# Kernel tuning notes

Measured on AMD Instinct MI355X. Metric: run time of the kernel, lower is better.

Reference implementation:

```python
import jax, jax.numpy as jnp
import numpy as np

# Static multi-scale feature pyramid shapes (value_shapes arg of MSDeformAttn.forward)
VALUE_SHAPES = ((80, 80), (40, 40), (20, 20), (10, 10))
N_HEADS, N_LEVELS, N_POINTS, D_MODEL = 8, 4, 4, 256


def setup_inputs() -> dict:
    key = jax.random.key(0)
    ks = jax.random.split(key, 11)
    bs, lq, d = 16, 1000, D_MODEL
    lv = sum(h * w for h, w in VALUE_SHAPES)  # 8500
    s = 0.02  # weight scale
    f32 = jnp.float32
    return {
        "query": jax.random.normal(ks[0], (bs, lq, d), f32),
        "refer_bbox": jax.random.uniform(ks[1], (bs, lq, 1, 4), f32),  # cxcywh in [0,1]
        "value": jax.random.normal(ks[2], (bs, lv, d), f32),
        "W_off": jax.random.normal(ks[3], (d, N_HEADS * N_LEVELS * N_POINTS * 2), f32) * s,
        "b_off": jax.random.normal(ks[4], (N_HEADS * N_LEVELS * N_POINTS * 2,), f32) * s,
        "W_attn": jax.random.normal(ks[5], (d, N_HEADS * N_LEVELS * N_POINTS), f32) * s,
        "b_attn": jax.random.normal(ks[6], (N_HEADS * N_LEVELS * N_POINTS,), f32) * s,
        "W_val": jax.random.normal(ks[7], (d, d), f32) * s,
        "b_val": jax.random.normal(ks[8], (d,), f32) * s,
        "W_out": jax.random.normal(ks[9], (d, d), f32) * s,
        "b_out": jax.random.normal(ks[10], (d,), f32) * s,
    }


def _bilinear_sample(v, x, y):
    """grid_sample(mode=bilinear, padding=zeros, align_corners=False) equivalent.
    v: [bs, H, W, nh, dh]; x, y: pixel-space coords [bs, lq, nh, P].
    Returns [bs, lq, nh, P, dh]."""
    bs, H, W, nh, dh = v.shape
    x0f = jnp.floor(x)
    y0f = jnp.floor(y)
    wx = x - x0f  # fractional weights
    wy = y - y0f
    x0 = x0f.astype(jnp.int32)
    y0 = y0f.astype(jnp.int32)
    x1, y1 = x0 + 1, y0 + 1
    b_idx = jnp.arange(bs)[:, None, None, None]
    h_idx = jnp.arange(nh)[None, None, :, None]

    def gather(yi, xi):
        valid = (xi >= 0) & (xi < W) & (yi >= 0) & (yi < H)
        xc = jnp.clip(xi, 0, W - 1)
        yc = jnp.clip(yi, 0, H - 1)
        val = v[b_idx, yc, xc, h_idx]  # [bs, lq, nh, P, dh]
        return val * valid[..., None].astype(v.dtype)

    return (gather(y0, x0) * ((1 - wx) * (1 - wy))[..., None]
            + gather(y0, x1) * (wx * (1 - wy))[..., None]
            + gather(y1, x0) * ((1 - wx) * wy)[..., None]
            + gather(y1, x1) * (wx * wy)[..., None])


def reference(query, refer_bbox, value, W_off, b_off, W_attn, b_attn, W_val, b_val, W_out, b_out):
    bs, lq, d = query.shape
    nh, L, P = N_HEADS, N_LEVELS, N_POINTS
    dh = d // nh

    # value projection
    v = value @ W_val + b_val  # [bs, lv, d]
    v = v.reshape(bs, -1, nh, dh)

    # sampling offsets and attention weights from query
    offsets = (query @ W_off + b_off).reshape(bs, lq, nh, L, P, 2)
    attn = (query @ W_attn + b_attn).reshape(bs, lq, nh, L * P)
    attn = jax.nn.softmax(attn, axis=-1).reshape(bs, lq, nh, L, P)

    # refer_bbox: [bs, lq, 1, 4] cxcywh; num_points == 4 branch
    add = offsets / P * refer_bbox[:, :, None, :, None, 2:] * 0.5
    loc = refer_bbox[:, :, None, :, None, :2] + add  # [bs, lq, nh, L, P, 2] in [0,1]

    out = jnp.zeros((bs, lq, nh, dh), query.dtype)
    start = 0
    for l, (H, W) in enumerate(VALUE_SHAPES):
        vl = v[:, start:start + H * W].reshape(bs, H, W, nh, dh)
        start += H * W
        ll = loc[:, :, :, l]  # [bs, lq, nh, P, 2]
        # normalized [0,1] -> pixel coords (align_corners=False): p = loc*size - 0.5
        x = ll[..., 0] * W - 0.5
        y = ll[..., 1] * H - 0.5
        sampled = _bilinear_sample(vl, x, y)  # [bs, lq, nh, P, dh]
        out = out + jnp.einsum('bqhpd,bqhp->bqhd', sampled, attn[:, :, :, l])

    out = out.reshape(bs, lq, d)
    return out @ W_out + b_out
```

## Files before the change

kernel.cpp:

```cpp
#include <hip/hip_runtime.h>
#include <cstdint>
#include <cstddef>


typedef unsigned short u16;
typedef u16 u16x8 __attribute__((ext_vector_type(8)));
typedef __bf16 bf16x8 __attribute__((ext_vector_type(8)));
typedef float f32x4 __attribute__((ext_vector_type(4)));

__device__ inline u16 f2bf(float f) {
  return __builtin_bit_cast(u16, (__bf16)f);
}

__device__ __forceinline__ void glds16(const void* g, void* l) {
  __builtin_amdgcn_global_load_lds(
      (const __attribute__((address_space(1))) void*)g,
      (__attribute__((address_space(3))) void*)l, 16, 0, 0);
}

__global__ __launch_bounds__(256) void wconv(
    const float* __restrict__ W0, const float* __restrict__ W1,
    const float* __restrict__ W2, const float* __restrict__ W3,
    u16* __restrict__ T0, u16* __restrict__ T1, u16* __restrict__ T2,
    u16* __restrict__ T3) {
  __shared__ u16 tile[64][65];
  const float* Ws[4] = {W0, W1, W2, W3};
  u16* Ts[4] = {T0, T1, T2, T3};
  const int Ns[4] = {256, 256, 128, 256};
  const int z = blockIdx.z;
  const int N = Ns[z];
  const int n0 = blockIdx.x * 64;
  if (n0 >= N) return;
  const int k0 = blockIdx.y * 64;
  const float* W = Ws[z];
  u16* Wt = Ts[z];
  const int tr = threadIdx.x >> 6;
  const int tc = threadIdx.x & 63;
#pragma unroll
  for (int r = 0; r < 64; r += 4)
    tile[r + tr][tc] = f2bf(W[(size_t)(k0 + r + tr) * N + n0 + tc]);
  __syncthreads();
#pragma unroll
  for (int r = 0; r < 64; r += 4)
    Wt[(size_t)(n0 + r + tr) * 256 + k0 + tc] = tile[tc][r + tr];
}

template <int WAVES, int NF, bool OUT_BF16>
__global__ __launch_bounds__(WAVES * 64, 1) void gemm_p2(
    const float* __restrict__ A, const u16* __restrict__ Wt,
    const float* __restrict__ bias, void* __restrict__ Cv,
    int M, int NT, int G) {
  constexpr int N = NF * 16;
  constexpr int TR = WAVES * 16;
  constexpr int STN = OUT_BF16 ? (NF / 2) : NF;
  __shared__ __align__(16) u16 Bls[N * 256];
  __shared__ __align__(16) float Asub[WAVES * 1024];
  const int wave = threadIdx.x >> 6;
  const int lane = threadIdx.x & 63;
  const int lr = lane & 15;
  const int lj = lane >> 4;

  constexpr int NI = NF * 8 / WAVES;
#pragma unroll
  for (int g = 0; g < NI; ++g) {
    int inst = wave * NI + g;
    int s2 = inst * 2 + (lane >> 5);
    int pc = lane & 31;
    int jc = pc ^ (s2 & 7);
    int c = (s2 & 15) * NF + (s2 >> 4);
    glds16((const char*)Wt + (size_t)c * 512 + (size_t)jc * 16,
           (char*)Bls + inst * 1024);
  }

  float bv[NF];
#pragma unroll
  for (int ni = 0; ni < NF; ++ni) bv[ni] = bias[lr * NF + ni];

  char* aw = (char*)Asub + wave * 4096;

  auto stageA = [&](int t, int s, int buf) {
#pragma unroll
    for (int i = 0; i < 2; ++i) {
      long row = (long)t * TR + wave * 16 + i * 8 + (lane >> 3);
      if (row > (long)M - 1) row = M - 1;
      int jc = (lane & 7) ^ (lane >> 3);
      glds16((const char*)A + row * 1024 + (size_t)s * 128 + (size_t)jc * 16,
             aw + buf * 2048 + i * 1024);
    }
  };

  stageA(blockIdx.x, 0, 0);
  stageA(blockIdx.x, 1, 1);
  __syncthreads();

  for (int t = blockIdx.x; t < NT; t += G) {
    f32x4 acc[NF] = {};
#pragma unroll
    for (int s = 0; s < 8; ++s) {
      if (s < 2) {
        if constexpr (STN == 8)
          asm volatile("s_waitcnt vmcnt(10)" ::: "memory");
        else
          asm volatile("s_waitcnt vmcnt(18)" ::: "memory");
      } else {
        asm volatile("s_waitcnt vmcnt(2)" ::: "memory");
      }
      const char* ab = aw + (s & 1) * 2048;
      const int sw = lr & 7;
      const int j0 = lj * 2;
      f32x4 a0 = *(const f32x4*)(ab + lr * 128 + ((j0 ^ sw) * 16));
      f32x4 a1 = *(const f32x4*)(ab + lr * 128 + (((j0 + 1) ^ sw) * 16));
      bf16x8 af;
      af[0] = (__bf16)a0[0]; af[1] = (__bf16)a0[1];
      af[2] = (__bf16)a0[2]; af[3] = (__bf16)a0[3];
      af[4] = (__bf16)a1[0]; af[5] = (__bf16)a1[1];
      af[6] = (__bf16)a1[2]; af[7] = (__bf16)a1[3];
#pragma unroll
      for (int ni = 0; ni < NF; ++ni) {
        int sl = ni * 16 + lr;
        int pc = (s * 4 + lj) ^ (sl & 7);
        bf16x8 b = __builtin_bit_cast(
            bf16x8, *(const u16x8*)((const char*)Bls + sl * 512 + pc * 16));
        acc[ni] = __builtin_amdgcn_mfma_f32_16x16x32_bf16(af, b, acc[ni],
                                                          0, 0, 0);
      }
      if (s < 6)
        stageA(t, s + 2, s & 1);
      else if (s == 6)
        stageA(t + G, 0, 0);
      else
        stageA(t + G, 1, 1);
    }
#pragma unroll
    for (int r = 0; r < 4; ++r) {
      long grow = (long)t * TR + wave * 16 + lj * 4 + r;
      if (grow >= M) continue;
      if (OUT_BF16) {
        bf16x8 lo, hi;
#pragma unroll
        for (int j = 0; j < 8; ++j) {
          lo[j] = (__bf16)(acc[j][r] + bv[j]);
          hi[j] = (__bf16)(acc[8 + j][r] + bv[8 + j]);
        }
        u16* pC = (u16*)Cv + grow * N + lr * NF;
        *(u16x8*)pC = __builtin_bit_cast(u16x8, lo);
        *(u16x8*)(pC + 8) = __builtin_bit_cast(u16x8, hi);
      } else {
#pragma unroll
        for (int q = 0; q < NF / 4; ++q) {
          f32x4 v;
#pragma unroll
          for (int j = 0; j < 4; ++j) v[j] = acc[q * 4 + j][r] + bv[q * 4 + j];
          *(f32x4*)((float*)Cv + grow * N + lr * NF + q * 4) = v;
        }
      }
    }
  }
}

__global__ __launch_bounds__(256, 4) void sample_fused(
    const float* __restrict__ Lgo, const float* __restrict__ Lga,
    const float* __restrict__ bbox, const u16* __restrict__ vbf,
    float* __restrict__ outs) {
  const int t = threadIdx.x;
  const int bi = blockIdx.x;
  const int xcd = bi & 7;
  const int j = bi >> 3;
  const int half = (j >= 125) ? 1 : 0;
  const int batch = xcd + 8 * half;
  const int qb = j - 125 * half;
  const int i0 = (batch * 125 + qb) * 8;

  __shared__ __align__(16) float sa[8 * 128];
  __shared__ __align__(16) int4 soff[1024];
  __shared__ __align__(16) float4 sw4[1024];
  __shared__ float sb[32];
  if (t < 32) sb[t] = bbox[(size_t)i0 * 4 + t];
  ((float4*)sa)[t] = ((const float4*)(Lga + (size_t)i0 * 128))[t];
  __syncthreads();
  if (t < 64) {
    int base = (t >> 3) * 128 + (t & 7) * 16;
    float mx = -3.0e38f;
#pragma unroll
    for (int k = 0; k < 16; ++k) mx = fmaxf(mx, sa[base + k]);
    float e[16];
    float s = 0.f;
#pragma unroll
    for (int k = 0; k < 16; ++k) {
      e[k] = __expf(sa[base + k] - mx);
      s += e[k];
    }
    float inv = 1.f / s;
#pragma unroll
    for (int k = 0; k < 16; ++k) sa[base + k] = e[k] * inv;
  }
  __syncthreads();
#pragma unroll
  for (int it = 0; it < 4; ++it) {
    int idx = it * 256 + t;
    int ql = idx >> 7;
    int rest = idx & 127;
    int h = rest >> 4;
    int pt = rest & 15;
    int l = pt >> 2;
    int W = 80 >> l;
    float offx = Lgo[(size_t)(i0 + ql) * 256 + h * 32 + pt * 2];
    float offy = Lgo[(size_t)(i0 + ql) * 256 + h * 32 + pt * 2 + 1];
    float xf = (sb[ql * 4 + 0] + offx * 0.125f * sb[ql * 4 + 2]) * (float)W - 0.5f;
    float yf = (sb[ql * 4 + 1] + offy * 0.125f * sb[ql * 4 + 3]) * (float)W - 0.5f;
    float aw = sa[ql * 128 + h * 16 + pt];
    float x0f = floorf(xf), y0f = floorf(yf);
    float wx = xf - x0f, wy = yf - y0f;
    int x0 = (int)x0f, y0 = (int)y0f;
    int x1 = x0 + 1, y1 = y0 + 1;
    float fx0 = (x0 >= 0 && x0 < W) ? 1.f : 0.f;
    float fx1 = (x1 >= 0 && x1 < W) ? 1.f : 0.f;
    float fy0 = (y0 >= 0 && y0 < W) ? 1.f : 0.f;
    float fy1 = (y1 >= 0 && y1 < W) ? 1.f : 0.f;
    int xc0 = min(max(x0, 0), W - 1), xc1 = min(max(x1, 0), W - 1);
    int yc0 = min(max(y0, 0), W - 1), yc1 = min(max(y1, 0), W - 1);
    int baseb = ((25600 - (25600 >> (2 * l))) / 3) * 512;
    int4 o;
    o.x = baseb + (yc0 * W + xc0) * 512;
    o.y = baseb + (yc0 * W + xc1) * 512;
    o.z = baseb + (yc1 * W + xc0) * 512;
    o.w = baseb + (yc1 * W + xc1) * 512;
    float aw0 = aw * (1.f - wy), aw1 = aw * wy;
    float4 wv;
    wv.x = aw0 * (1.f - wx) * fx0 * fy0;
    wv.y = aw0 * wx * fx1 * fy0;
    wv.z = aw1 * (1.f - wx) * fx0 * fy1;
    wv.w = aw1 * wx * fx1 * fy1;
    int phys = ql * 128 + h * 16 + (pt ^ h);
    soff[phys] = o;
    sw4[phys] = wv;
  }
  __syncthreads();
  const int ql = t >> 5;
  const int r = t & 31;
  const int h = r >> 2;
  const int cg = r & 3;
  const int chb = (h * 32 + cg * 8) * 2;
  const char* vbb = (const char*)vbf + (size_t)batch * 8500 * 512 + chb;
  float acc[8] = {};
#pragma unroll 2
  for (int pt = 0; pt < 16; ++pt) {
    int phys = ql * 128 + h * 16 + (pt ^ h);
    int4 o = soff[phys];
    float4 wv = sw4[phys];
    uint4 v00 = *(const uint4*)(vbb + o.x);
    uint4 v01 = *(const uint4*)(vbb + o.y);
    uint4 v10 = *(const uint4*)(vbb + o.z);
    uint4 v11 = *(const uint4*)(vbb + o.w);
    const uint32_t* p00 = (const uint32_t*)&v00;
    const uint32_t* p01 = (const uint32_t*)&v01;
    const uint32_t* p10 = (const uint32_t*)&v10;
    const uint32_t* p11 = (const uint32_t*)&v11;
#pragma unroll
    for (int k = 0; k < 4; ++k) {
      float a0 = __uint_as_float(p00[k] << 16);
      float a1 = __uint_as_float(p00[k] & 0xffff0000u);
      float b0 = __uint_as_float(p01[k] << 16);
      float b1 = __uint_as_float(p01[k] & 0xffff0000u);
      float c0 = __uint_as_float(p10[k] << 16);
      float c1 = __uint_as_float(p10[k] & 0xffff0000u);
      float d0 = __uint_as_float(p11[k] << 16);
      float d1 = __uint_as_float(p11[k] & 0xffff0000u);
      acc[2 * k] += wv.x * a0 + wv.y * b0 + wv.z * c0 + wv.w * d0;
      acc[2 * k + 1] += wv.x * a1 + wv.y * b1 + wv.z * c1 + wv.w * d1;
    }
  }
  float4* op = (float4*)(outs + (size_t)(i0 + ql) * 256 + h * 32 + cg * 8);
  op[0] = make_float4(acc[0], acc[1], acc[2], acc[3]);
  op[1] = make_float4(acc[4], acc[5], acc[6], acc[7]);
}

extern "C" void kernel_launch(void* const* d_in, const int* in_sizes, int n_in,
                              void* d_out, int out_size, void* d_ws, size_t ws_size,
                              hipStream_t stream) {
  const float* query  = (const float*)d_in[0];
  const float* bbox   = (const float*)d_in[1];
  const float* value  = (const float*)d_in[2];
  const float* W_off  = (const float*)d_in[3];
  const float* b_off  = (const float*)d_in[4];
  const float* W_attn = (const float*)d_in[5];
  const float* b_attn = (const float*)d_in[6];
  const float* W_val  = (const float*)d_in[7];
  const float* b_val  = (const float*)d_in[8];
  const float* W_out  = (const float*)d_in[9];
  const float* b_out  = (const float*)d_in[10];
  float* out = (float*)d_out;

  char* w = (char*)d_ws;
  u16* vbf     = (u16*)w;
  float* Lgo   = (float*)(w + 69632000);
  float* Lga   = (float*)(w + 86016000);
  float* outs  = (float*)(w + 94208000);
  u16* Wt_val  = (u16*)(w + 110592000);
  u16* Wt_off  = (u16*)(w + 110723072);
  u16* Wt_attn = (u16*)(w + 110854144);
  u16* Wt_out  = (u16*)(w + 110919680);

  const int M_v = 16 * 8500;
  const int M_q = 16 * 1000;

  wconv<<<dim3(4, 4, 4), 256, 0, stream>>>(W_val, W_off, W_attn, W_out,
                                           Wt_val, Wt_off, Wt_attn, Wt_out);
  gemm_p2<8, 16, true><<<256, 512, 0, stream>>>(
      value, Wt_val, b_val, (void*)vbf, M_v, 1063, 256);
  gemm_p2<4, 16, false><<<250, 256, 0, stream>>>(
      query, Wt_off, b_off, (void*)Lgo, M_q, 250, 250);
  gemm_p2<4, 8, false><<<250, 256, 0, stream>>>(
      query, Wt_attn, b_attn, (void*)Lga, M_q, 250, 250);
  sample_fused<<<2000, 256, 0, stream>>>(Lgo, Lga, bbox, vbf, outs);
  gemm_p2<4, 16, false><<<250, 256, 0, stream>>>(
      outs, Wt_out, b_out, (void*)out, M_q, 250, 250);
}
```

Measured before the change: 124.7 us.

## Add register double-buffered persistent GEMM for value projection

```diff
diff --git a/kernel.cpp b/kernel.cpp
--- a/kernel.cpp
+++ b/kernel.cpp
@@ -43,6 +43,95 @@
 #pragma unroll
   for (int r = 0; r < 64; r += 4)
     Wt[(size_t)(n0 + r + tr) * 256 + k0 + tc] = tile[tc][r + tr];
+}
+
+__global__ __launch_bounds__(512, 1) void gemm_p3(
+    const float* __restrict__ A, const u16* __restrict__ Wt,
+    const float* __restrict__ bias, u16* __restrict__ Cv,
+    int M, int NT, int G) {
+  __shared__ __align__(16) u16 Bls[256 * 256];
+  const int wave = threadIdx.x >> 6;
+  const int lane = threadIdx.x & 63;
+  const int lr = lane & 15;
+  const int lj = lane >> 4;
+
+#pragma unroll
+  for (int g = 0; g < 16; ++g) {
+    int inst = wave * 16 + g;
+    int s2 = inst * 2 + (lane >> 5);
+    int pc = lane & 31;
+    int jc = pc ^ (s2 & 7);
+    int c = (s2 & 15) * 16 + (s2 >> 4);
+    glds16((const char*)Wt + (size_t)c * 512 + (size_t)jc * 16,
+           (char*)Bls + inst * 1024);
+  }
+
+  float bv[16];
+#pragma unroll
+  for (int ni = 0; ni < 16; ++ni) bv[ni] = bias[lr * 16 + ni];
+
+  f32x4 bufA[16], bufB[16];
+
+  auto loadT = [&](f32x4 (&buf)[16], int t) {
+    long row = (long)t * 128 + wave * 16 + lr;
+    if (row > (long)M - 1) row = M - 1;
+    const float* ap = A + row * 256 + lj * 8;
+#pragma unroll
+    for (int s = 0; s < 8; ++s) {
+      buf[s * 2 + 0] = *(const f32x4*)(ap + s * 32);
+      buf[s * 2 + 1] = *(const f32x4*)(ap + s * 32 + 4);
+    }
+  };
+
+  auto compT = [&](const f32x4 (&buf)[16], int t) {
+    if (t >= NT) return;
+    f32x4 acc[16] = {};
+#pragma unroll
+    for (int s = 0; s < 8; ++s) {
+      bf16x8 af;
+      af[0] = (__bf16)buf[s * 2][0];
+      af[1] = (__bf16)buf[s * 2][1];
+      af[2] = (__bf16)buf[s * 2][2];
+      af[3] = (__bf16)buf[s * 2][3];
+      af[4] = (__bf16)buf[s * 2 + 1][0];
+      af[5] = (__bf16)buf[s * 2 + 1][1];
+      af[6] = (__bf16)buf[s * 2 + 1][2];
+      af[7] = (__bf16)buf[s * 2 + 1][3];
+#pragma unroll
+      for (int ni = 0; ni < 16; ++ni) {
+        int sl = ni * 16 + lr;
+        int pc = (s * 4 + lj) ^ (sl & 7);
+        bf16x8 b = __builtin_bit_cast(
+            bf16x8, *(const u16x8*)((const char*)Bls + sl * 512 + pc * 16));
+        acc[ni] = __builtin_amdgcn_mfma_f32_16x16x32_bf16(af, b, acc[ni],
+                                                          0, 0, 0);
+      }
+    }
+#pragma unroll
+    for (int r = 0; r < 4; ++r) {
+      long grow = (long)t * 128 + wave * 16 + lj * 4 + r;
+      if (grow >= M) continue;
+      bf16x8 lo, hi;
+#pragma unroll
+      for (int j = 0; j < 8; ++j) {
+        lo[j] = (__bf16)(acc[j][r] + bv[j]);
+        hi[j] = (__bf16)(acc[8 + j][r] + bv[8 + j]);
+      }
+      u16* pC = Cv + grow * 256 + lr * 16;
+      *(u16x8*)pC = __builtin_bit_cast(u16x8, lo);
+      *(u16x8*)(pC + 8) = __builtin_bit_cast(u16x8, hi);
+    }
+  };
+
+  loadT(bufA, blockIdx.x);
+  loadT(bufB, blockIdx.x + G);
+  __syncthreads();
+  for (int t = blockIdx.x; t < NT; t += 2 * G) {
+    compT(bufA, t);
+    loadT(bufA, t + 2 * G);
+    compT(bufB, t + G);
+    loadT(bufB, t + 3 * G);
+  }
 }
 
 template <int WAVES, int NF, bool OUT_BF16>
@@ -306,8 +395,7 @@
 
   wconv<<<dim3(4, 4, 4), 256, 0, stream>>>(W_val, W_off, W_attn, W_out,
                                            Wt_val, Wt_off, Wt_attn, Wt_out);
-  gemm_p2<8, 16, true><<<256, 512, 0, stream>>>(
-      value, Wt_val, b_val, (void*)vbf, M_v, 1063, 256);
+  gemm_p3<<<256, 512, 0, stream>>>(value, Wt_val, b_val, vbf, M_v, 1063, 256);
   gemm_p2<4, 16, false><<<250, 256, 0, stream>>>(
       query, Wt_off, b_off, (void*)Lgo, M_q, 250, 250);
   gemm_p2<4, 8, false><<<250, 256, 0, stream>>>(
```

Result: slower. 333.1 us (+167.1%).
